# Optimization experiments

Measured on AMD Instinct MI355X. Metric: run time of the kernel, lower is better.

The kernel has to match this reference:

```python
import jax, jax.numpy as jnp
import numpy as np

B, N, C, H = 8, 4096, 512, 8
HD = C // H  # head_dim = 64
SCALE = HD ** -0.5


def setup_inputs() -> dict:
    key = jax.random.key(0)
    k1, k2, k3, k4 = jax.random.split(key, 4)
    x1 = jax.random.normal(k1, (B, N, C), dtype=jnp.float32)
    x2 = jax.random.normal(k2, (B, N, C), dtype=jnp.float32)
    # nn.Linear(dim, 2*dim, bias=False) weights; stored as [in, out] for x @ W
    lim = 1.0 / np.sqrt(C)
    W_kv1 = jax.random.uniform(k3, (C, 2 * C), dtype=jnp.float32, minval=-lim, maxval=lim)
    W_kv2 = jax.random.uniform(k4, (C, 2 * C), dtype=jnp.float32, minval=-lim, maxval=lim)
    return {"x1": x1, "x2": x2, "W_kv1": W_kv1, "W_kv2": W_kv2}


def _heads(t):
    # [B, N, C] -> [B, H, N, HD]
    return t.reshape(B, N, H, HD).transpose(0, 2, 1, 3)


def _kv(x, W):
    kv = (x @ W).reshape(B, N, 2, H, HD)  # [B, N, 2, H, HD]
    kv = kv.transpose(2, 0, 3, 1, 4)      # [2, B, H, N, HD]
    return kv[0], kv[1]


def _ctx(k, v):
    # K^T V: [B, H, HD, HD], scaled then softmax over axis -2 (the k-feature axis)
    ctx = jnp.einsum("bhnd,bhne->bhde", k, v) * SCALE
    return jax.nn.softmax(ctx, axis=-2)


def reference(x1, x2, W_kv1, W_kv2):
    q1 = _heads(x1)
    q2 = _heads(x2)
    k1, v1 = _kv(x1, W_kv1)
    k2, v2 = _kv(x2, W_kv2)
    ctx1 = _ctx(k1, v1)
    ctx2 = _ctx(k2, v2)
    # cross: q1 attends via ctx2, q2 via ctx1
    o1 = jnp.einsum("bhnd,bhde->bhne", q1, ctx2).transpose(0, 2, 1, 3).reshape(B, N, C)
    o2 = jnp.einsum("bhnd,bhde->bhne", q2, ctx1).transpose(0, 2, 1, 3).reshape(B, N, C)
    return o1, o2
```

## Files before the change

kernel.cpp:

```cpp
#include <hip/hip_runtime.h>
#include <stdint.h>
#include <stddef.h>

#define NB 8
#define NSEQ 4096
#define NC 512
#define NH 8
#define SWZ(c) ((((c) >> 2) ^ (c)) & 7)

typedef __attribute__((ext_vector_type(4))) float f4;
typedef __attribute__((ext_vector_type(8))) short bf8;
typedef __attribute__((ext_vector_type(4))) short bf4;
typedef __attribute__((ext_vector_type(2))) unsigned int u32x2;
typedef __attribute__((ext_vector_type(4))) unsigned int u32x4;

__device__ __forceinline__ short f2bf(float f) {
  union { float f; unsigned int u; } v; v.f = f;
  unsigned int u = v.u + 0x7FFFu + ((v.u >> 16) & 1u);
  return (short)(u >> 16);
}
__device__ __forceinline__ float bf2f(short h) {
  union { unsigned int u; float f; } v;
  v.u = ((unsigned int)(unsigned short)h) << 16;
  return v.f;
}
__device__ __forceinline__ unsigned int cvtpk(float a, float b) {
  unsigned int r;
  asm("v_cvt_pk_bf16_f32 %0, %1, %2" : "=v"(r) : "v"(a), "v"(b));
  return r;
}

__global__ __launch_bounds__(256) void k_wt(const float* __restrict__ W0,
                                            const float* __restrict__ W1,
                                            short* __restrict__ Wth,
                                            short* __restrict__ Wtl) {
  __shared__ float t[64 * 65];
  int bid = blockIdx.x;
  int ot = bid & 15;
  int ct = (bid >> 4) & 7;
  int s = bid >> 7;
  const float* W = s ? W1 : W0;
  const float* src = W + (size_t)(ct * 64) * 1024 + ot * 64;
  int tid = threadIdx.x;
  int rr = tid >> 4, c4 = (tid & 15) * 4;
#pragma unroll
  for (int p = 0; p < 4; ++p) {
    int c = p * 16 + rr;
    f4 v = *(const f4*)&src[(size_t)c * 1024 + c4];
#pragma unroll
    for (int i = 0; i < 4; ++i) t[(c4 + i) * 65 + c] = v[i];
  }
  __syncthreads();
  size_t obase = (size_t)s * 524288 + (size_t)(ot * 64) * 512 + ct * 64;
#pragma unroll
  for (int p = 0; p < 4; ++p) {
    int o = p * 16 + rr;
    bf4 vh, vl;
#pragma unroll
    for (int i = 0; i < 4; ++i) {
      float v = t[o * 65 + c4 + i];
      short h = f2bf(v);
      vh[i] = h; vl[i] = f2bf(v - bf2f(h));
    }
    *(bf4*)&Wth[obase + (size_t)o * 512 + c4] = vh;
    *(bf4*)&Wtl[obase + (size_t)o * 512 + c4] = vl;
  }
}

__global__ __launch_bounds__(256) void k_gram(const float* __restrict__ x0,
                                              const float* __restrict__ x1,
                                              float* __restrict__ G32a,
                                              float* __restrict__ G32b) {
  __shared__ short Ab[64 * 64];
  __shared__ short Bb[64 * 64];
  int bid = blockIdx.x;
  int xcd = bid & 7;
  int j = bid >> 3;
  int kh = j >= 72;
  int jj = j - kh * 72;
  int sb = xcd + ((jj >= 36) ? 8 : 0);
  int p = (jj >= 36) ? (jj - 36) : jj;
  int ti = 0;
  while (p >= 8 - ti) { p -= 8 - ti; ++ti; }
  int tj = ti + p;
  int diag = (ti == tj);
  int s = sb >> 3, b = sb & 7;
  const float* x = s ? x1 : x0;
  const float* Axp = x + (size_t)b * NSEQ * NC + (size_t)kh * 2048 * NC + ti * 64;
  const float* Bxp = x + (size_t)b * NSEQ * NC + (size_t)kh * 2048 * NC + tj * 64;
  int tid = threadIdx.x;
  int lane = tid & 63;
  int w = tid >> 6;
  int c4 = (tid & 15) * 4;
  int n4 = (tid >> 4) * 4;
  int g = n4 >> 3;
  int nlo = n4 & 7;
  int wr = w & 1, wc = w >> 1;
  int mrow = lane & 15;
  int kreg = lane >> 4;
  f4 z = {0.f, 0.f, 0.f, 0.f};
  f4 acc[2][2];
#pragma unroll
  for (int i = 0; i < 2; ++i)
#pragma unroll
    for (int jq = 0; jq < 2; ++jq) acc[i][jq] = z;

  f4 va[4], vb[4];
  auto load = [&](int n0) {
#pragma unroll
    for (int i = 0; i < 4; ++i)
      va[i] = *(const f4*)&Axp[(size_t)(n0 + n4 + i) * NC + c4];
    if (!diag) {
#pragma unroll
      for (int i = 0; i < 4; ++i)
        vb[i] = *(const f4*)&Bxp[(size_t)(n0 + n4 + i) * NC + c4];
    }
  };
  auto store = [&]() {
#pragma unroll
    for (int ci = 0; ci < 4; ++ci) {
      int c = c4 + ci;
      int soff = c * 64 + ((g ^ SWZ(c)) << 3) + nlo;
      u32x2 wa;
      wa[0] = cvtpk(va[0][ci], va[1][ci]);
      wa[1] = cvtpk(va[2][ci], va[3][ci]);
      *(u32x2*)&Ab[soff] = wa;
      if (!diag) {
        u32x2 wb;
        wb[0] = cvtpk(vb[0][ci], vb[1][ci]);
        wb[1] = cvtpk(vb[2][ci], vb[3][ci]);
        *(u32x2*)&Bb[soff] = wb;
      }
    }
  };
  auto comp = [&]() {
    const short* Bbuf = diag ? Ab : Bb;
#pragma unroll
    for (int kk = 0; kk < 2; ++kk) {
      int gr = kk * 4 + kreg;
      bf8 a[2], bb[2];
#pragma unroll
      for (int i = 0; i < 2; ++i) {
        int ra = wr * 32 + i * 16 + mrow;
        a[i] = *(const bf8*)&Ab[ra * 64 + ((gr ^ SWZ(ra)) << 3)];
        int rb2 = wc * 32 + i * 16 + mrow;
        bb[i] = *(const bf8*)&Bbuf[rb2 * 64 + ((gr ^ SWZ(rb2)) << 3)];
      }
#pragma unroll
      for (int i = 0; i < 2; ++i)
#pragma unroll
        for (int jq = 0; jq < 2; ++jq)
          acc[i][jq] = __builtin_amdgcn_mfma_f32_16x16x32_bf16(a[i], bb[jq], acc[i][jq], 0, 0, 0);
    }
  };

  load(0);
  for (int it = 0; it < 32; ++it) {
    store();
    __syncthreads();
    if (it < 31) load((it + 1) * 64);
    __builtin_amdgcn_sched_barrier(0);
    comp();
    __syncthreads();
  }

  float* Gp = (kh ? G32b : G32a) + (size_t)sb * NC * NC;
  int rb = ti * 64 + wr * 32 + (lane >> 4) * 4;
  int cb = tj * 64 + wc * 32 + (lane & 15);
#pragma unroll
  for (int i = 0; i < 2; ++i)
#pragma unroll
    for (int jq = 0; jq < 2; ++jq)
#pragma unroll
      for (int r = 0; r < 4; ++r)
        Gp[(size_t)(rb + i * 16 + r) * NC + cb + jq * 16] = acc[i][jq][r];
}

__global__ __launch_bounds__(256) void k_sym(const float* __restrict__ G32a,
                                             const float* __restrict__ G32b,
                                             short* __restrict__ Gh,
                                             short* __restrict__ Gl) {
  __shared__ float t[64 * 65];
  int bid = blockIdx.x;
  int tile = bid & 63;
  int sb = bid >> 6;
  int ti = tile >> 3, tj = tile & 7;
  int tr = ti > tj;
  size_t soff = (size_t)sb * 262144
              + (tr ? ((size_t)(tj * 64) * 512 + ti * 64)
                    : ((size_t)(ti * 64) * 512 + tj * 64));
  const float* srcA = G32a + soff;
  const float* srcB = G32b + soff;
  int tid = threadIdx.x;
  int rr = tid >> 4;
  int c4 = (tid & 15) * 4;
#pragma unroll
  for (int p = 0; p < 4; ++p) {
    int r = p * 16 + rr;
    f4 v = *(const f4*)&srcA[(size_t)r * 512 + c4];
    f4 v2 = *(const f4*)&srcB[(size_t)r * 512 + c4];
    v += v2;
    if (tr) {
#pragma unroll
      for (int i = 0; i < 4; ++i) t[(c4 + i) * 65 + r] = v[i];
    } else {
#pragma unroll
      for (int i = 0; i < 4; ++i) t[r * 65 + c4 + i] = v[i];
    }
  }
  __syncthreads();
  size_t obase = (size_t)sb * 262144 + (size_t)(ti * 64) * 512 + tj * 64;
#pragma unroll
  for (int p = 0; p < 4; ++p) {
    int r = p * 16 + rr;
    bf4 vh, vl;
#pragma unroll
    for (int i = 0; i < 4; ++i) {
      float v = t[r * 65 + c4 + i] * 0.125f;
      short h = f2bf(v);
      vh[i] = h; vl[i] = f2bf(v - bf2f(h));
    }
    *(bf4*)&Gh[obase + (size_t)r * 512 + c4] = vh;
    *(bf4*)&Gl[obase + (size_t)r * 512 + c4] = vl;
  }
}

__global__ __launch_bounds__(256) void k_t(const short* __restrict__ Wth,
                                           const short* __restrict__ Wtl,
                                           const short* __restrict__ Gh,
                                           const short* __restrict__ Gl,
                                           float* __restrict__ Ttf) {
  __shared__ short Ah[128 * 40];
  __shared__ short Al[128 * 40];
  __shared__ short Bh[128 * 40];
  __shared__ short Bl[128 * 40];
  int tid = threadIdx.x;
  int et = blockIdx.x & 3;
  int ct = blockIdx.x >> 2;
  int sb = blockIdx.y;
  int s = sb >> 3;
  const short* Avh = Wth + ((size_t)s * 1024 + 512 + (size_t)et * 128) * NC;
  const short* Avl = Wtl + ((size_t)s * 1024 + 512 + (size_t)et * 128) * NC;
  const short* Gph = Gh + (size_t)sb * 262144 + (size_t)(ct * 128) * 512;
  const short* Gpl = Gl + (size_t)sb * 262144 + (size_t)(ct * 128) * 512;
  int cc = tid >> 1;
  int kh = (tid & 1) * 16;
  int lane = tid & 63;
  int w = tid >> 6;
  int wm = (w & 1) * 64;
  int wn = (w >> 1) * 64;
  int mrow = lane & 15;
  int kcol = (lane >> 4) * 8;
  f4 z = {0.f, 0.f, 0.f, 0.f};
  f4 acc[4][4];
#pragma unroll
  for (int i = 0; i < 4; ++i)
#pragma unroll
    for (int j = 0; j < 4; ++j) acc[i][j] = z;

  for (int it = 0; it < 16; ++it) {
    int k0 = it * 32;
    __syncthreads();
    *(bf8*)&Ah[cc * 40 + kh]     = *(const bf8*)&Avh[(size_t)cc * NC + k0 + kh];
    *(bf8*)&Ah[cc * 40 + kh + 8] = *(const bf8*)&Avh[(size_t)cc * NC + k0 + kh + 8];
    *(bf8*)&Al[cc * 40 + kh]     = *(const bf8*)&Avl[(size_t)cc * NC + k0 + kh];
    *(bf8*)&Al[cc * 40 + kh + 8] = *(const bf8*)&Avl[(size_t)cc * NC + k0 + kh + 8];
    *(bf8*)&Bh[cc * 40 + kh]     = *(const bf8*)&Gph[(size_t)cc * 512 + k0 + kh];
    *(bf8*)&Bh[cc * 40 + kh + 8] = *(const bf8*)&Gph[(size_t)cc * 512 + k0 + kh + 8];
    *(bf8*)&Bl[cc * 40 + kh]     = *(const bf8*)&Gpl[(size_t)cc * 512 + k0 + kh];
    *(bf8*)&Bl[cc * 40 + kh + 8] = *(const bf8*)&Gpl[(size_t)cc * 512 + k0 + kh + 8];
    __syncthreads();
    bf8 ah[4], al[4], bh[4], bl[4];
#pragma unroll
    for (int i = 0; i < 4; ++i) {
      ah[i] = *(const bf8*)&Ah[(wm + i * 16 + mrow) * 40 + kcol];
      al[i] = *(const bf8*)&Al[(wm + i * 16 + mrow) * 40 + kcol];
      bh[i] = *(const bf8*)&Bh[(wn + i * 16 + mrow) * 40 + kcol];
      bl[i] = *(const bf8*)&Bl[(wn + i * 16 + mrow) * 40 + kcol];
    }
#pragma unroll
    for (int i = 0; i < 4; ++i)
#pragma unroll
      for (int j = 0; j < 4; ++j) {
        acc[i][j] = __builtin_amdgcn_mfma_f32_16x16x32_bf16(ah[i], bh[j], acc[i][j], 0, 0, 0);
        acc[i][j] = __builtin_amdgcn_mfma_f32_16x16x32_bf16(ah[i], bl[j], acc[i][j], 0, 0, 0);
        acc[i][j] = __builtin_amdgcn_mfma_f32_16x16x32_bf16(al[i], bh[j], acc[i][j], 0, 0, 0);
      }
  }
  float* Tp = Ttf + (size_t)sb * NC * NC;
  int rb = et * 128 + wm + (lane >> 4) * 4;
  int cb = ct * 128 + wn + (lane & 15);
#pragma unroll
  for (int i = 0; i < 4; ++i)
#pragma unroll
    for (int j = 0; j < 4; ++j)
#pragma unroll
      for (int r = 0; r < 4; ++r)
        Tp[(size_t)(rb + i * 16 + r) * NC + cb + j * 16] = acc[i][j][r];
}

__global__ __launch_bounds__(256) void k_ctx(const short* __restrict__ Wth,
                                             const short* __restrict__ Wtl,
                                             const float* __restrict__ Ttf,
                                             short* __restrict__ ctxT) {
  __shared__ short Ah[64 * 72];
  __shared__ short Al[64 * 72];
  __shared__ short Bh[64 * 72];
  __shared__ short Bl[64 * 72];
  __shared__ float Sf[64 * 68];
  int tid = threadIdx.x;
  int h = blockIdx.x & 7;
  int sb = blockIdx.x >> 3;
  int s = sb >> 3;
  const short* Akh = Wth + ((size_t)s * 1024 + (size_t)h * 64) * NC;
  const short* Akl = Wtl + ((size_t)s * 1024 + (size_t)h * 64) * NC;
  const float* Bt = Ttf + ((size_t)sb * NC + (size_t)h * 64) * NC;
  int cs = tid >> 3;
  int kg = (tid & 7) * 8;
  int lane = tid & 63;
  int w = tid >> 6;
  int mrow = lane & 15;
  int kcol = (lane >> 4) * 8;
  f4 z = {0.f, 0.f, 0.f, 0.f};
  f4 acc[4];
#pragma unroll
  for (int j = 0; j < 4; ++j) acc[j] = z;

  for (int it = 0; it < 8; ++it) {
    int k0 = it * 64;
    __syncthreads();
#pragma unroll
    for (int r = 0; r < 2; ++r) {
      int d = cs + r * 32;
      *(bf8*)&Ah[d * 72 + kg] = *(const bf8*)&Akh[(size_t)d * NC + k0 + kg];
      *(bf8*)&Al[d * 72 + kg] = *(const bf8*)&Akl[(size_t)d * NC + k0 + kg];
      f4 g0 = *(const f4*)&Bt[(size_t)d * NC + k0 + kg];
      f4 g1 = *(const f4*)&Bt[(size_t)d * NC + k0 + kg + 4];
      bf8 vh, vl;
#pragma unroll
      for (int i = 0; i < 4; ++i) {
        short hh = f2bf(g0[i]);
        vh[i] = hh; vl[i] = f2bf(g0[i] - bf2f(hh));
        hh = f2bf(g1[i]);
        vh[i + 4] = hh; vl[i + 4] = f2bf(g1[i] - bf2f(hh));
      }
      *(bf8*)&Bh[d * 72 + kg] = vh;
      *(bf8*)&Bl[d * 72 + kg] = vl;
    }
    __syncthreads();
#pragma unroll
    for (int kk = 0; kk < 2; ++kk) {
      bf8 ah = *(const bf8*)&Ah[(w * 16 + mrow) * 72 + kk * 32 + kcol];
      bf8 al = *(const bf8*)&Al[(w * 16 + mrow) * 72 + kk * 32 + kcol];
#pragma unroll
      for (int j = 0; j < 4; ++j) {
        bf8 bh = *(const bf8*)&Bh[(j * 16 + mrow) * 72 + kk * 32 + kcol];
        bf8 bl = *(const bf8*)&Bl[(j * 16 + mrow) * 72 + kk * 32 + kcol];
        acc[j] = __builtin_amdgcn_mfma_f32_16x16x32_bf16(ah, bh, acc[j], 0, 0, 0);
        acc[j] = __builtin_amdgcn_mfma_f32_16x16x32_bf16(ah, bl, acc[j], 0, 0, 0);
        acc[j] = __builtin_amdgcn_mfma_f32_16x16x32_bf16(al, bh, acc[j], 0, 0, 0);
      }
    }
  }
  __syncthreads();
#pragma unroll
  for (int j = 0; j < 4; ++j)
#pragma unroll
    for (int r = 0; r < 4; ++r)
      Sf[(w * 16 + (lane >> 4) * 4 + r) * 68 + j * 16 + (lane & 15)] = acc[j][r];
  __syncthreads();
  if (tid < 64) {
    int e = tid;
    float mx = -1e30f;
    for (int d = 0; d < 64; ++d) mx = fmaxf(mx, Sf[d * 68 + e]);
    float sum = 0.f;
    for (int d = 0; d < 64; ++d) {
      float ev = __expf(Sf[d * 68 + e] - mx);
      sum += ev;
      Sf[d * 68 + e] = ev;
    }
    float rs = 1.f / sum;
    short* cp = ctxT + (((size_t)sb * NH + h) * 64 + e) * 64;
    for (int d0 = 0; d0 < 64; d0 += 4) {
      bf4 ov;
      ov[0] = f2bf(Sf[(d0 + 0) * 68 + e] * rs);
      ov[1] = f2bf(Sf[(d0 + 1) * 68 + e] * rs);
      ov[2] = f2bf(Sf[(d0 + 2) * 68 + e] * rs);
      ov[3] = f2bf(Sf[(d0 + 3) * 68 + e] * rs);
      *(bf4*)&cp[d0] = ov;
    }
  }
}

__global__ __launch_bounds__(256) void k_o(const float* __restrict__ x0,
                                           const float* __restrict__ x1,
                                           const short* __restrict__ ctxT,
                                           float* __restrict__ out) {
  __shared__ short Ab[128 * 72];
  __shared__ short Bb[64 * 72];
  int tid = threadIdx.x;
  int bx = blockIdx.x;
  int nt = bx & 31;
  int h = (bx >> 5) & 7;
  int b = (bx >> 8) & 7;
  int so = bx >> 11;
  const float* x = so ? x1 : x0;
  const short* cp = ctxT + (((size_t)(1 - so) * NB + b) * NH + h) * 64 * 64;
  {
    int e = tid >> 2;
    int dg = (tid & 3) * 16;
    *(bf8*)&Bb[e * 72 + dg] = *(const bf8*)&cp[e * 64 + dg];
    *(bf8*)&Bb[e * 72 + dg + 8] = *(const bf8*)&cp[e * 64 + dg + 8];
  }
  const float* xp = x + ((size_t)b * NSEQ + (size_t)nt * 128) * NC + h * 64;
  {
    int n = tid >> 1;
    int dh = (tid & 1) * 32;
    const float* row = xp + (size_t)n * NC + dh;
#pragma unroll
    for (int q = 0; q < 4; ++q) {
      f4 v0 = *(const f4*)&row[q * 8];
      f4 v1 = *(const f4*)&row[q * 8 + 4];
      u32x4 pw;
      pw[0] = cvtpk(v0[0], v0[1]);
      pw[1] = cvtpk(v0[2], v0[3]);
      pw[2] = cvtpk(v1[0], v1[1]);
      pw[3] = cvtpk(v1[2], v1[3]);
      *(u32x4*)&Ab[n * 72 + dh + q * 8] = pw;
    }
  }
  __syncthreads();
  int lane = tid & 63;
  int w = tid >> 6;
  int mrow = lane & 15;
  int kcol = (lane >> 4) * 8;
  f4 z = {0.f, 0.f, 0.f, 0.f};
  f4 acc[2][4];
#pragma unroll
  for (int i = 0; i < 2; ++i)
#pragma unroll
    for (int j = 0; j < 4; ++j) acc[i][j] = z;
#pragma unroll
  for (int kk = 0; kk < 2; ++kk) {
    bf8 a0 = *(const bf8*)&Ab[(w * 32 + mrow) * 72 + kk * 32 + kcol];
    bf8 a1 = *(const bf8*)&Ab[(w * 32 + 16 + mrow) * 72 + kk * 32 + kcol];
#pragma unroll
    for (int j = 0; j < 4; ++j) {
      bf8 bv = *(const bf8*)&Bb[(j * 16 + mrow) * 72 + kk * 32 + kcol];
      acc[0][j] = __builtin_amdgcn_mfma_f32_16x16x32_bf16(a0, bv, acc[0][j], 0, 0, 0);
      acc[1][j] = __builtin_amdgcn_mfma_f32_16x16x32_bf16(a1, bv, acc[1][j], 0, 0, 0);
    }
  }
  float* op = out + (size_t)so * ((size_t)NB * NSEQ * NC)
            + ((size_t)b * NSEQ + (size_t)nt * 128) * NC + h * 64;
#pragma unroll
  for (int i = 0; i < 2; ++i)
#pragma unroll
    for (int j = 0; j < 4; ++j)
#pragma unroll
      for (int r = 0; r < 4; ++r)
        op[(size_t)(w * 32 + i * 16 + (lane >> 4) * 4 + r) * NC + j * 16 + (lane & 15)] = acc[i][j][r];
}

extern "C" void kernel_launch(void* const* d_in, const int* in_sizes, int n_in,
                              void* d_out, int out_size, void* d_ws, size_t ws_size,
                              hipStream_t stream) {
  const float* x1 = (const float*)d_in[0];
  const float* x2 = (const float*)d_in[1];
  const float* W1 = (const float*)d_in[2];
  const float* W2 = (const float*)d_in[3];
  float* out = (float*)d_out;
  char* ws = (char*)d_ws;
  float* Ttf  = (float*)ws;
  short* Gh   = (short*)(ws + 16777216);
  short* Gl   = (short*)(ws + 25165824);
  float* G32a = (float*)(ws + 33554432);
  float* G32b = (float*)(ws + 50331648);
  short* Wth  = (short*)(ws + 67108864);
  short* Wtl  = (short*)(ws + 69206016);
  short* ctxT = (short*)(ws + 71303168);

  hipLaunchKernelGGL(k_wt,   dim3(256),    dim3(256), 0, stream, W1, W2, Wth, Wtl);
  hipLaunchKernelGGL(k_gram, dim3(1152),   dim3(256), 0, stream, x1, x2, G32a, G32b);
  hipLaunchKernelGGL(k_sym,  dim3(1024),   dim3(256), 0, stream, G32a, G32b, Gh, Gl);
  hipLaunchKernelGGL(k_t,    dim3(16, 16), dim3(256), 0, stream, Wth, Wtl, Gh, Gl, Ttf);
  hipLaunchKernelGGL(k_ctx,  dim3(128),    dim3(256), 0, stream, Wth, Wtl, Ttf, ctxT);
  hipLaunchKernelGGL(k_o,    dim3(4096),   dim3(256), 0, stream, x1, x2, ctxT, out);
}
```

Measured before the change: 166.6 us.

## Double the K-chunk per iteration in gram kernel and use inline-asm global loads

The gram (x^T x) kernel now stages 128 sequence rows per iteration instead of 64. This halves the number of barrier-separated iterations and doubles the loads in flight per thread. Global loads are issued through inline asm, with explicit vmcnt/lgkmcnt waits and raw s_barrier calls in place of __syncthreads. The cost is twice the LDS (32 KB) and more registers for the staged f4 values, which may lower occupancy.

```diff
diff --git a/kernel.cpp b/kernel.cpp
--- a/kernel.cpp
+++ b/kernel.cpp
@@ -71,8 +71,8 @@
                                               const float* __restrict__ x1,
                                               float* __restrict__ G32a,
                                               float* __restrict__ G32b) {
-  __shared__ short Ab[64 * 64];
-  __shared__ short Bb[64 * 64];
+  __shared__ short bfA[64 * 128];
+  __shared__ short bfB[64 * 128];
   int bid = blockIdx.x;
   int xcd = bid & 7;
   int j = bid >> 3;
@@ -93,8 +93,6 @@
   int w = tid >> 6;
   int c4 = (tid & 15) * 4;
   int n4 = (tid >> 4) * 4;
-  int g = n4 >> 3;
-  int nlo = n4 & 7;
   int wr = w & 1, wc = w >> 1;
   int mrow = lane & 15;
   int kreg = lane >> 4;
@@ -105,46 +103,61 @@
 #pragma unroll
     for (int jq = 0; jq < 2; ++jq) acc[i][jq] = z;
 
-  f4 va[4], vb[4];
-  auto load = [&](int n0) {
-#pragma unroll
-    for (int i = 0; i < 4; ++i)
-      va[i] = *(const f4*)&Axp[(size_t)(n0 + n4 + i) * NC + c4];
+  f4 va[8], vb[8];
+  auto load = [&](int k0) {
+#pragma unroll
+    for (int gq = 0; gq < 2; ++gq)
+#pragma unroll
+      for (int i = 0; i < 4; ++i) {
+        const float* pa = Axp + (size_t)(k0 + gq * 64 + n4 + i) * NC + c4;
+        asm volatile("global_load_dwordx4 %0, %1, off"
+                     : "=v"(va[gq * 4 + i]) : "v"(pa));
+      }
     if (!diag) {
 #pragma unroll
-      for (int i = 0; i < 4; ++i)
-        vb[i] = *(const f4*)&Bxp[(size_t)(n0 + n4 + i) * NC + c4];
+      for (int gq = 0; gq < 2; ++gq)
+#pragma unroll
+        for (int i = 0; i < 4; ++i) {
+          const float* pb = Bxp + (size_t)(k0 + gq * 64 + n4 + i) * NC + c4;
+          asm volatile("global_load_dwordx4 %0, %1, off"
+                       : "=v"(vb[gq * 4 + i]) : "v"(pb));
+        }
     }
   };
   auto store = [&]() {
 #pragma unroll
-    for (int ci = 0; ci < 4; ++ci) {
-      int c = c4 + ci;
-      int soff = c * 64 + ((g ^ SWZ(c)) << 3) + nlo;
-      u32x2 wa;
-      wa[0] = cvtpk(va[0][ci], va[1][ci]);
-      wa[1] = cvtpk(va[2][ci], va[3][ci]);
-      *(u32x2*)&Ab[soff] = wa;
-      if (!diag) {
-        u32x2 wb;
-        wb[0] = cvtpk(vb[0][ci], vb[1][ci]);
-        wb[1] = cvtpk(vb[2][ci], vb[3][ci]);
-        *(u32x2*)&Bb[soff] = wb;
+    for (int gq = 0; gq < 2; ++gq)
+#pragma unroll
+      for (int ci = 0; ci < 4; ++ci) {
+        int c = c4 + ci;
+        int slot = gq * 8 + (((n4 >> 3) ^ SWZ(c)) & 7);
+        int soff = c * 128 + slot * 8 + (n4 & 7);
+        u32x2 wa;
+        wa[0] = cvtpk(va[gq * 4 + 0][ci], va[gq * 4 + 1][ci]);
+        wa[1] = cvtpk(va[gq * 4 + 2][ci], va[gq * 4 + 3][ci]);
+        *(u32x2*)&bfA[soff] = wa;
+        if (!diag) {
+          u32x2 wb;
+          wb[0] = cvtpk(vb[gq * 4 + 0][ci], vb[gq * 4 + 1][ci]);
+          wb[1] = cvtpk(vb[gq * 4 + 2][ci], vb[gq * 4 + 3][ci]);
+          *(u32x2*)&bfB[soff] = wb;
+        }
       }
-    }
   };
   auto comp = [&]() {
-    const short* Bbuf = diag ? Ab : Bb;
-#pragma unroll
-    for (int kk = 0; kk < 2; ++kk) {
+    const short* Bbuf = diag ? bfA : bfB;
+#pragma unroll
+    for (int kk = 0; kk < 4; ++kk) {
       int gr = kk * 4 + kreg;
       bf8 a[2], bb[2];
 #pragma unroll
       for (int i = 0; i < 2; ++i) {
         int ra = wr * 32 + i * 16 + mrow;
-        a[i] = *(const bf8*)&Ab[ra * 64 + ((gr ^ SWZ(ra)) << 3)];
+        int sa = (gr & 8) | ((gr ^ SWZ(ra)) & 7);
+        a[i] = *(const bf8*)&bfA[ra * 128 + sa * 8];
         int rb2 = wc * 32 + i * 16 + mrow;
-        bb[i] = *(const bf8*)&Bbuf[rb2 * 64 + ((gr ^ SWZ(rb2)) << 3)];
+        int sb2 = (gr & 8) | ((gr ^ SWZ(rb2)) & 7);
+        bb[i] = *(const bf8*)&Bbuf[rb2 * 128 + sb2 * 8];
       }
 #pragma unroll
       for (int i = 0; i < 2; ++i)
@@ -155,13 +168,19 @@
   };
 
   load(0);
-  for (int it = 0; it < 32; ++it) {
+  for (int it = 0; it < 16; ++it) {
+    asm volatile("s_waitcnt vmcnt(0)" ::: "memory");
+    __builtin_amdgcn_sched_barrier(0);
     store();
-    __syncthreads();
-    if (it < 31) load((it + 1) * 64);
+    asm volatile("s_waitcnt lgkmcnt(0)" ::: "memory");
+    __builtin_amdgcn_sched_barrier(0);
+    __builtin_amdgcn_s_barrier();
+    if (it < 15) load((it + 1) * 128);
     __builtin_amdgcn_sched_barrier(0);
     comp();
-    __syncthreads();
+    asm volatile("s_waitcnt lgkmcnt(0)" ::: "memory");
+    __builtin_amdgcn_sched_barrier(0);
+    __builtin_amdgcn_s_barrier();
   }
 
   float* Gp = (kh ? G32b : G32a) + (size_t)sb * NC * NC;
```

After: 167.0 us. About the same (+0.2%).
